# Kernel tuning notes

Hardware: AMD Instinct MI355X
Metric: run time of the kernel (lower is better)

The kernel has to match this reference:

```python
import jax, jax.numpy as jnp
import numpy as np

DIM = 1024
HEADS = 16
DIM_HEAD = 64
INNER = HEADS * DIM_HEAD  # 1024
MAX_POS = 512
B, N = 2, 1024


def setup_inputs() -> dict:
    key = jax.random.key(0)
    ks = jax.random.split(key, 6)
    s = DIM ** -0.5
    x = jax.random.normal(ks[0], (B, N, DIM), dtype=jnp.float32)
    Wq = jax.random.normal(ks[1], (DIM, INNER), dtype=jnp.float32) * s
    Wkv = jax.random.normal(ks[2], (DIM, 2 * INNER), dtype=jnp.float32) * s
    Wo = jax.random.normal(ks[3], (INNER, DIM), dtype=jnp.float32) * (INNER ** -0.5)
    bo = jnp.zeros((DIM,), dtype=jnp.float32)
    rel_emb = jax.random.normal(ks[4], (2 * MAX_POS + 1, DIM_HEAD), dtype=jnp.float32)
    return {"x": x, "Wq": Wq, "Wkv": Wkv, "Wo": Wo, "bo": bo, "rel_emb": rel_emb}


def reference(x, Wq, Wkv, Wo, bo, rel_emb):
    b, n, _ = x.shape
    scale = DIM_HEAD ** -0.5
    q = x @ Wq                    # [b, n, inner]
    kv = x @ Wkv                  # [b, n, 2*inner]
    k, v = jnp.split(kv, 2, axis=-1)

    def split_heads(t):
        return t.reshape(b, n, HEADS, DIM_HEAD).transpose(0, 2, 1, 3)  # [b,h,n,d]

    q, k, v = map(split_heads, (q, k, v))
    dots = jnp.einsum('bhid,bhjd->bhij', q, k) * scale

    seq = jnp.arange(n)
    dist = jnp.clip(seq[:, None] - seq[None, :], -MAX_POS, MAX_POS) + MAX_POS  # [n, n]
    rel = rel_emb[dist]           # [n, n, d]
    pos_attn = jnp.einsum('bhnd,nrd->bhnr', q, rel) * scale
    dots = dots + pos_attn

    attn = jax.nn.softmax(dots, axis=-1)
    out = jnp.einsum('bhij,bhjd->bhid', attn, v)
    out = out.transpose(0, 2, 1, 3).reshape(b, n, INNER)
    return out @ Wo + bo
```

## Files before the change

kernel.cpp:

```cpp
#include <hip/hip_runtime.h>

typedef __bf16 bf16x8 __attribute__((ext_vector_type(8)));
typedef float f32x4 __attribute__((ext_vector_type(4)));

#define DEV __device__ __forceinline__

DEV unsigned short f2bf(float f) {
  union { float f; unsigned u; } x; x.f = f;
  unsigned r = x.u + 0x7FFFu + ((x.u >> 16) & 1u);
  return (unsigned short)(r >> 16);
}
DEV float bf2f(unsigned short h) {
  union { unsigned u; float f; } x; x.u = ((unsigned)h) << 16;
  return x.f;
}

typedef __attribute__((address_space(3))) void* lds_vp;
typedef const __attribute__((address_space(1))) void* gbl_vp;
DEV void load_lds16(const unsigned short* gp, void* lp) {
  __builtin_amdgcn_global_load_lds((gbl_vp)(const void*)gp, (lds_vp)lp, 16, 0, 0);
}

__global__ __launch_bounds__(256)
void prep_k(const float* __restrict__ x, const float* __restrict__ rel,
            const float* __restrict__ bo, const float* __restrict__ Wq,
            const float* __restrict__ Wkv, const float* __restrict__ Wo,
            unsigned short* __restrict__ xb, unsigned short* __restrict__ relb,
            unsigned short* __restrict__ bob, unsigned short* __restrict__ WqkvT,
            unsigned short* __restrict__ WoT) {
  __shared__ unsigned short tile[32][33];
  const int bid = blockIdx.x, tid = threadIdx.x;
  if (bid < 2114) {
    const float* src; unsigned short* dst; long base; long n;
    if (bid < 2048)      { src = x;   dst = xb;   base = (long)bid * 1024;          n = 2097152; }
    else if (bid < 2113) { src = rel; dst = relb; base = (long)(bid - 2048) * 1024; n = 65600; }
    else                 { src = bo;  dst = bob;  base = 0;                          n = 1024; }
    long i = base + tid * 4;
    if (i < n) {
      float4 v = *(const float4*)&src[i];
      unsigned long long u = (unsigned long long)f2bf(v.x)
                           | ((unsigned long long)f2bf(v.y) << 16)
                           | ((unsigned long long)f2bf(v.z) << 32)
                           | ((unsigned long long)f2bf(v.w) << 48);
      *(unsigned long long*)&dst[i] = u;
    }
  } else {
    int id = bid - 2114;
    const float* src; unsigned short* dst; const int R = 1024; int C, txt, tyt;
    if (id < 1024)      { src = Wq;  dst = WqkvT;           C = 1024; txt = id & 31; tyt = id >> 5; }
    else if (id < 3072) { int l = id - 1024; src = Wkv; dst = WqkvT + 1048576; C = 2048; txt = l & 63; tyt = l >> 6; }
    else                { int l = id - 3072; src = Wo;  dst = WoT;             C = 1024; txt = l & 31; tyt = l >> 5; }
    int c0 = txt * 32, r0 = tyt * 32;
    int tx = tid & 31, ty = tid >> 5;
    #pragma unroll
    for (int i = 0; i < 4; ++i)
      tile[ty + i * 8][tx] = f2bf(src[(size_t)(r0 + ty + i * 8) * C + c0 + tx]);
    __syncthreads();
    #pragma unroll
    for (int i = 0; i < 4; ++i)
      dst[(size_t)(c0 + ty + i * 8) * R + r0 + tx] = tile[tx][ty + i * 8];
  }
}

__global__ __launch_bounds__(256)
void gemm_qkv(const unsigned short* __restrict__ A,
              const unsigned short* __restrict__ Bt,
              unsigned short* __restrict__ o0,
              unsigned short* __restrict__ o1,
              unsigned short* __restrict__ o2) {
  __shared__ __align__(16) unsigned short As[128][32];
  __shared__ __align__(16) unsigned short Bs[128][32];
  const int tid  = threadIdx.x;
  const int lane = tid & 63, wave = tid >> 6;
  const int q15  = lane & 15, quad = lane >> 4;
  const int wr = wave >> 1, wc = wave & 1;
  const int m0 = blockIdx.y * 128, n0 = blockIdx.x * 128;
  const int K = 1024;
  const int lrow = lane >> 2, lkc = (lane & 3) * 8;

  f32x4 acc[4][4] = {};
  for (int k0 = 0; k0 < K; k0 += 32) {
    __syncthreads();
    #pragma unroll
    for (int t = 0; t < 2; ++t) {
      int r0 = wave * 32 + t * 16;
      load_lds16(&A[(size_t)(m0 + r0 + lrow) * K + k0 + lkc], &As[r0][0]);
      load_lds16(&Bt[(size_t)(n0 + r0 + lrow) * K + k0 + lkc], &Bs[r0][0]);
    }
    __syncthreads();
    bf16x8 af[4], bfr[4];
    #pragma unroll
    for (int i = 0; i < 4; ++i) {
      af[i]  = *(const bf16x8*)&As[wr * 64 + i * 16 + q15][quad * 8];
      bfr[i] = *(const bf16x8*)&Bs[wc * 64 + i * 16 + q15][quad * 8];
    }
    #pragma unroll
    for (int i = 0; i < 4; ++i)
      #pragma unroll
      for (int j = 0; j < 4; ++j)
        acc[i][j] = __builtin_amdgcn_mfma_f32_16x16x32_bf16(af[i], bfr[j], acc[i][j], 0, 0, 0);
  }
  #pragma unroll
  for (int i = 0; i < 4; ++i)
    #pragma unroll
    for (int j = 0; j < 4; ++j)
      #pragma unroll
      for (int r = 0; r < 4; ++r) {
        int row = m0 + wr * 64 + i * 16 + quad * 4 + r;
        int col = n0 + wc * 64 + j * 16 + q15;
        float v = acc[i][j][r];
        int b = row >> 10, nn = row & 1023;
        unsigned short* dst; int c = col; float sc = 1.f;
        if (col < 1024)      { dst = o0; sc = 0.125f; }
        else if (col < 2048) { dst = o1; c = col - 1024; }
        else                 { dst = o2; c = col - 2048; }
        int h = c >> 6, dd = c & 63;
        dst[((size_t)(b * 16 + h) * 1024 + nn) * 64 + dd] = f2bf(v * sc);
      }
}

__global__ __launch_bounds__(256)
void transpose_v_k(const unsigned short* __restrict__ v,
                   unsigned short* __restrict__ vt) {
  __shared__ __align__(16) unsigned short st[64][68];
  const int bh = blockIdx.y, n0 = blockIdx.x * 64;
  const unsigned short* vp = v + (size_t)bh * 1024 * 64;
  unsigned short* tp = vt + (size_t)bh * 64 * 1024;
  #pragma unroll
  for (int cc = 0; cc < 2; ++cc) {
    int ci = threadIdx.x + cc * 256;
    int row = ci >> 3, dc = (ci & 7) * 8;
    *(uint4*)&st[row][dc] = *(const uint4*)&vp[(size_t)(n0 + row) * 64 + dc];
  }
  __syncthreads();
  #pragma unroll
  for (int cc = 0; cc < 2; ++cc) {
    int ci = threadIdx.x + cc * 256;
    int d = ci >> 3, nc = (ci & 7) * 8;
    union { uint4 v; unsigned short us[8]; } t;
    #pragma unroll
    for (int e = 0; e < 8; ++e) t.us[e] = st[nc + e][d];
    *(uint4*)&tp[(size_t)d * 1024 + n0 + nc] = t.v;
  }
}

DEV void stage16(const unsigned short* gbase, size_t gstride,
                 unsigned short* lbase, int r0, int lane) {
  #pragma unroll
  for (int t = 0; t < 2; ++t) {
    int r = r0 + t * 8 + (lane >> 3);
    int lc = (lane & 7) ^ (r & 7);
    load_lds16(&gbase[(size_t)r * gstride + lc * 8], &lbase[(size_t)(r0 + t * 8) * 64]);
  }
}
DEV bf16x8 read_swz(const unsigned short* buf, int row, int lc) {
  int pc = lc ^ (row & 7);
  return *(const bf16x8*)&buf[row * 64 + pc * 8];
}

__global__ __launch_bounds__(256)
void flash_attn(const unsigned short* __restrict__ q_ws,
                const unsigned short* __restrict__ k_ws,
                const unsigned short* __restrict__ vt_ws,
                const unsigned short* __restrict__ rel,
                unsigned short* __restrict__ Opart,
                float* __restrict__ lpart) {
  __shared__ __align__(16) unsigned short Kbuf[2][64 * 64];
  __shared__ __align__(16) unsigned short Vbuf[2][64 * 64];
  __shared__ __align__(16) unsigned short P_lds[4][16 * 64];

  const int tid  = threadIdx.x;
  const int lane = tid & 63, w = tid >> 6;
  const int q15  = lane & 15, quad = lane >> 4;
  const int bh = blockIdx.x;
  const int it = blockIdx.y >> 1, sp = blockIdx.y & 1;
  const int ib = it * 64 + w * 16;
  const int jbase = sp * 512;

  const unsigned short* qp = q_ws  + (size_t)bh * 1024 * 64;
  const unsigned short* kp = k_ws  + (size_t)bh * 1024 * 64;
  const unsigned short* tp = vt_ws + (size_t)bh * 64 * 1024;

  bf16x8 aq[2];
  #pragma unroll
  for (int ks = 0; ks < 2; ++ks)
    aq[ks] = *(const bf16x8*)&qp[(size_t)(ib + q15) * 64 + ks * 32 + quad * 8];

  f32x4 o[4] = {};
  float l_i[4] = {0.f, 0.f, 0.f, 0.f};

  stage16(kp + (size_t)jbase * 64, 64, &Kbuf[0][0], w * 16, lane);
  stage16(tp + jbase, 1024, &Vbuf[0][0], w * 16, lane);

  for (int jt = 0; jt < 8; ++jt) {
    const int j0 = jbase + jt * 64, cur = jt & 1;
    __syncthreads();
    if (jt + 1 < 8) {
      stage16(kp + (size_t)(j0 + 64) * 64, 64, &Kbuf[cur ^ 1][0], w * 16, lane);
      stage16(tp + (j0 + 64), 1024, &Vbuf[cur ^ 1][0], w * 16, lane);
    }

    f32x4 accS[4] = {};
    #pragma unroll
    for (int ks = 0; ks < 2; ++ks)
      #pragma unroll
      for (int cb = 0; cb < 4; ++cb) {
        bf16x8 bk = read_swz(&Kbuf[cur][0], cb * 16 + q15, ks * 4 + quad);
        accS[cb] = __builtin_amdgcn_mfma_f32_16x16x32_bf16(aq[ks], bk, accS[cb], 0, 0, 0);
      }
    int tb = ib - j0 + 512 - 63;
    f32x4 accT[5] = {};
    #pragma unroll
    for (int ks = 0; ks < 2; ++ks)
      #pragma unroll
      for (int ub = 0; ub < 5; ++ub) {
        int trow = tb + ub * 16 + q15;
        trow = trow < 0 ? 0 : (trow > 1024 ? 1024 : trow);
        bf16x8 br = *(const bf16x8*)&rel[(size_t)trow * 64 + ks * 32 + quad * 8];
        accT[ub] = __builtin_amdgcn_mfma_f32_16x16x32_bf16(aq[ks], br, accT[ub], 0, 0, 0);
      }

    #pragma unroll
    for (int r = 0; r < 4; ++r) {
      const int dl = quad * 4 + r;
      const int src = quad * 16 + ((15 + dl - q15) & 15);
      float tv[5];
      #pragma unroll
      for (int ub = 0; ub < 5; ++ub)
        tv[ub] = __shfl(accT[ub][r], src, 64);
      const bool hi = (q15 < dl);
      #pragma unroll
      for (int cb = 0; cb < 4; ++cb) {
        float tval = hi ? tv[4 - cb] : tv[3 - cb];
        float s = accS[cb][r] + tval;
        float p = exp2f(s * 1.44269504f - 64.f);
        l_i[r] += p;
        int k = cb * 16 + q15;
        P_lds[w][dl * 64 + ((((k >> 3) ^ (dl & 7)) << 3) | (k & 7))] = f2bf(p);
      }
    }

    #pragma unroll
    for (int ks = 0; ks < 2; ++ks) {
      bf16x8 ap = *(const bf16x8*)&P_lds[w][q15 * 64 + (((ks * 4 + quad) ^ (q15 & 7)) << 3)];
      #pragma unroll
      for (int db = 0; db < 4; ++db) {
        bf16x8 bv = read_swz(&Vbuf[cur][0], db * 16 + q15, ks * 4 + quad);
        o[db] = __builtin_amdgcn_mfma_f32_16x16x32_bf16(ap, bv, o[db], 0, 0, 0);
      }
    }
  }

  #pragma unroll
  for (int r = 0; r < 4; ++r)
    #pragma unroll
    for (int off = 1; off < 16; off <<= 1)
      l_i[r] += __shfl_xor(l_i[r], off, 64);

  unsigned short* op = Opart + ((size_t)sp * 32 + bh) * 1024 * 64;
  #pragma unroll
  for (int db = 0; db < 4; ++db)
    #pragma unroll
    for (int r = 0; r < 4; ++r) {
      int row = ib + quad * 4 + r;
      op[(size_t)row * 64 + db * 16 + q15] = f2bf(o[db][r]);
    }
  if (q15 == 0)
    #pragma unroll
    for (int r = 0; r < 4; ++r)
      lpart[(size_t)sp * 32768 + bh * 1024 + ib + quad * 4 + r] = l_i[r];
}

__global__ __launch_bounds__(256)
void combine_k(const unsigned short* __restrict__ Opart,
               const float* __restrict__ lpart,
               unsigned short* __restrict__ ao) {
  int e = (blockIdx.x * 256 + threadIdx.x) * 4;
  if (e >= 2097152) return;
  int bh = e >> 16, rem = e & 65535, row = rem >> 6, d = e & 63;
  size_t off = (size_t)bh * 65536 + rem;
  const unsigned short* p0 = Opart + off;
  const unsigned short* p1 = Opart + 2097152 + off;
  float li = 1.f / (lpart[bh * 1024 + row] + lpart[32768 + bh * 1024 + row] + 1e-30f);
  ushort2 a0 = *(const ushort2*)p0, a1 = *(const ushort2*)(p0 + 2);
  ushort2 b0 = *(const ushort2*)p1, b1 = *(const ushort2*)(p1 + 2);
  int b = bh >> 4, h = bh & 15;
  unsigned short* dst = ao + ((size_t)(b * 1024 + row)) * 1024 + h * 64 + d;
  dst[0] = f2bf((bf2f(a0.x) + bf2f(b0.x)) * li);
  dst[1] = f2bf((bf2f(a0.y) + bf2f(b0.y)) * li);
  dst[2] = f2bf((bf2f(a1.x) + bf2f(b1.x)) * li);
  dst[3] = f2bf((bf2f(a1.y) + bf2f(b1.y)) * li);
}

__global__ __launch_bounds__(256)
void gemm_out(const unsigned short* __restrict__ A,
              const unsigned short* __restrict__ Bt,
              const unsigned short* __restrict__ bias,
              float* __restrict__ fo) {
  __shared__ __align__(16) unsigned short As[128][32];
  __shared__ __align__(16) unsigned short Bs[64][32];
  const int tid  = threadIdx.x;
  const int lane = tid & 63, w = tid >> 6;
  const int q15  = lane & 15, quad = lane >> 4;
  const int m0 = blockIdx.y * 128, n0 = blockIdx.x * 64;
  const int K = 1024, N = 1024;
  const int lrow = lane >> 2, lkc = (lane & 3) * 8;

  f32x4 acc[2][4] = {};
  for (int k0 = 0; k0 < K; k0 += 32) {
    __syncthreads();
    #pragma unroll
    for (int t = 0; t < 2; ++t) {
      int r0 = w * 32 + t * 16;
      load_lds16(&A[(size_t)(m0 + r0 + lrow) * K + k0 + lkc], &As[r0][0]);
    }
    load_lds16(&Bt[(size_t)(n0 + w * 16 + lrow) * K + k0 + lkc], &Bs[w * 16][0]);
    __syncthreads();
    bf16x8 af[2], bfr[4];
    #pragma unroll
    for (int i = 0; i < 2; ++i)
      af[i] = *(const bf16x8*)&As[w * 32 + i * 16 + q15][quad * 8];
    #pragma unroll
    for (int j = 0; j < 4; ++j)
      bfr[j] = *(const bf16x8*)&Bs[j * 16 + q15][quad * 8];
    #pragma unroll
    for (int i = 0; i < 2; ++i)
      #pragma unroll
      for (int j = 0; j < 4; ++j)
        acc[i][j] = __builtin_amdgcn_mfma_f32_16x16x32_bf16(af[i], bfr[j], acc[i][j], 0, 0, 0);
  }
  #pragma unroll
  for (int i = 0; i < 2; ++i)
    #pragma unroll
    for (int j = 0; j < 4; ++j)
      #pragma unroll
      for (int r = 0; r < 4; ++r) {
        int row = m0 + w * 32 + i * 16 + quad * 4 + r;
        int col = n0 + j * 16 + q15;
        fo[(size_t)row * N + col] = acc[i][j][r] + bf2f(bias[col]);
      }
}

extern "C" void kernel_launch(void* const* d_in, const int* in_sizes, int n_in,
                              void* d_out, int out_size, void* d_ws, size_t ws_size,
                              hipStream_t stream) {
  (void)in_sizes; (void)n_in; (void)out_size; (void)ws_size;
  const float* x   = (const float*)d_in[0];
  const float* Wq  = (const float*)d_in[1];
  const float* Wkv = (const float*)d_in[2];
  const float* Wo  = (const float*)d_in[3];
  const float* bo  = (const float*)d_in[4];
  const float* rel = (const float*)d_in[5];
  float* out = (float*)d_out;

  unsigned short* ws = (unsigned short*)d_ws;
  unsigned short* WoT   = ws;
  unsigned short* relb  = WoT   + 1048576;
  unsigned short* bob   = relb  + 65664;
  unsigned short* q_ws  = bob   + 1088;
  unsigned short* k_ws  = q_ws  + 2097152;
  unsigned short* vT    = k_ws  + 2097152;
  unsigned short* WqkvT = vT    + 2097152;
  unsigned short* xb    = WqkvT + 3145728;
  unsigned short* v_row = xb    + 2097152;
  float*          lpart = (float*)(v_row + 2097152);
  unsigned short* Opart = WqkvT;
  unsigned short* ao    = v_row;

  prep_k<<<6210, 256, 0, stream>>>(x, rel, bo, Wq, Wkv, Wo,
                                   xb, relb, bob, WqkvT, WoT);
  gemm_qkv<<<dim3(24, 16), 256, 0, stream>>>(xb, WqkvT, q_ws, k_ws, v_row);
  transpose_v_k<<<dim3(16, 32), 256, 0, stream>>>(v_row, vT);
  flash_attn<<<dim3(32, 32), 256, 0, stream>>>(q_ws, k_ws, vT, relb, Opart, lpart);
  combine_k<<<2048, 256, 0, stream>>>(Opart, lpart, ao);
  gemm_out<<<dim3(16, 16), 256, 0, stream>>>(ao, WoT, bob, out);
}
```

Measured before the change: 189.6 us.

## Fuse V transpose into QKV GEMM epilogue and drop split-KV combine pass

The QKV GEMM epilogue now transposes V tiles through LDS and writes V^T directly, which removes the separate transpose kernel and the row-major V buffer. Flash attention no longer splits the key range in two. Each block loops over all 16 key tiles, normalizes by the row sum, and writes the merged head-interleaved output directly. This eliminates the combine kernel and the partial output and sum-buffer traffic. In exchange the attention grid shrinks to half as many blocks, each doing twice the sequential work, which reduces parallelism on the GPU.

```diff
diff --git a/kernel.cpp b/kernel.cpp
--- a/kernel.cpp
+++ b/kernel.cpp
@@ -70,6 +70,7 @@
               unsigned short* __restrict__ o2) {
   __shared__ __align__(16) unsigned short As[128][32];
   __shared__ __align__(16) unsigned short Bs[128][32];
+  __shared__ unsigned short tbuf[128][68];
   const int tid  = threadIdx.x;
   const int lane = tid & 63, wave = tid >> 6;
   const int q15  = lane & 15, quad = lane >> 4;
@@ -100,47 +101,53 @@
       for (int j = 0; j < 4; ++j)
         acc[i][j] = __builtin_amdgcn_mfma_f32_16x16x32_bf16(af[i], bfr[j], acc[i][j], 0, 0, 0);
   }
-  #pragma unroll
-  for (int i = 0; i < 4; ++i)
-    #pragma unroll
-    for (int j = 0; j < 4; ++j)
-      #pragma unroll
-      for (int r = 0; r < 4; ++r) {
-        int row = m0 + wr * 64 + i * 16 + quad * 4 + r;
-        int col = n0 + wc * 64 + j * 16 + q15;
-        float v = acc[i][j][r];
-        int b = row >> 10, nn = row & 1023;
-        unsigned short* dst; int c = col; float sc = 1.f;
-        if (col < 1024)      { dst = o0; sc = 0.125f; }
-        else if (col < 2048) { dst = o1; c = col - 1024; }
-        else                 { dst = o2; c = col - 2048; }
-        int h = c >> 6, dd = c & 63;
-        dst[((size_t)(b * 16 + h) * 1024 + nn) * 64 + dd] = f2bf(v * sc);
-      }
-}
-
-__global__ __launch_bounds__(256)
-void transpose_v_k(const unsigned short* __restrict__ v,
-                   unsigned short* __restrict__ vt) {
-  __shared__ __align__(16) unsigned short st[64][68];
-  const int bh = blockIdx.y, n0 = blockIdx.x * 64;
-  const unsigned short* vp = v + (size_t)bh * 1024 * 64;
-  unsigned short* tp = vt + (size_t)bh * 64 * 1024;
-  #pragma unroll
-  for (int cc = 0; cc < 2; ++cc) {
-    int ci = threadIdx.x + cc * 256;
-    int row = ci >> 3, dc = (ci & 7) * 8;
-    *(uint4*)&st[row][dc] = *(const uint4*)&vp[(size_t)(n0 + row) * 64 + dc];
-  }
-  __syncthreads();
-  #pragma unroll
-  for (int cc = 0; cc < 2; ++cc) {
-    int ci = threadIdx.x + cc * 256;
-    int d = ci >> 3, nc = (ci & 7) * 8;
-    union { uint4 v; unsigned short us[8]; } t;
-    #pragma unroll
-    for (int e = 0; e < 8; ++e) t.us[e] = st[nc + e][d];
-    *(uint4*)&tp[(size_t)d * 1024 + n0 + nc] = t.v;
+
+  const int b = m0 >> 10, nn0 = m0 & 1023;
+  if (n0 < 2048) {
+    #pragma unroll
+    for (int i = 0; i < 4; ++i)
+      #pragma unroll
+      for (int j = 0; j < 4; ++j)
+        #pragma unroll
+        for (int r = 0; r < 4; ++r) {
+          int row = m0 + wr * 64 + i * 16 + quad * 4 + r;
+          int col = n0 + wc * 64 + j * 16 + q15;
+          float v = acc[i][j][r];
+          int nn = row & 1023;
+          unsigned short* dst; int c = col; float sc = 1.f;
+          if (col < 1024) { dst = o0; sc = 0.125f; }
+          else            { dst = o1; c = col - 1024; }
+          int h = c >> 6, dd = c & 63;
+          dst[((size_t)((row >> 10) * 16 + h) * 1024 + nn) * 64 + dd] = f2bf(v * sc);
+        }
+  } else {
+    const int hp = (n0 - 2048) >> 6;
+    #pragma unroll
+    for (int hh = 0; hh < 2; ++hh) {
+      __syncthreads();
+      if (wc == hh) {
+        #pragma unroll
+        for (int i = 0; i < 4; ++i)
+          #pragma unroll
+          for (int j = 0; j < 4; ++j)
+            #pragma unroll
+            for (int r = 0; r < 4; ++r)
+              tbuf[wr * 64 + i * 16 + quad * 4 + r][j * 16 + q15] = f2bf(acc[i][j][r]);
+      }
+      __syncthreads();
+      const int bh = b * 16 + hp + hh;
+      const int dl = tid >> 3, nb = (tid & 7) * 8;
+      #pragma unroll
+      for (int p = 0; p < 2; ++p)
+        #pragma unroll
+        for (int s = 0; s < 2; ++s) {
+          int d = dl + p * 32, n = nb + s * 64;
+          union { uint4 v; unsigned short us[8]; } t;
+          #pragma unroll
+          for (int e = 0; e < 8; ++e) t.us[e] = tbuf[n + e][d];
+          *(uint4*)&o2[((size_t)bh * 64 + d) * 1024 + nn0 + n] = t.v;
+        }
+    }
   }
 }
 
@@ -163,8 +170,7 @@
                 const unsigned short* __restrict__ k_ws,
                 const unsigned short* __restrict__ vt_ws,
                 const unsigned short* __restrict__ rel,
-                unsigned short* __restrict__ Opart,
-                float* __restrict__ lpart) {
+                unsigned short* __restrict__ ao) {
   __shared__ __align__(16) unsigned short Kbuf[2][64 * 64];
   __shared__ __align__(16) unsigned short Vbuf[2][64 * 64];
   __shared__ __align__(16) unsigned short P_lds[4][16 * 64];
@@ -173,9 +179,7 @@
   const int lane = tid & 63, w = tid >> 6;
   const int q15  = lane & 15, quad = lane >> 4;
   const int bh = blockIdx.x;
-  const int it = blockIdx.y >> 1, sp = blockIdx.y & 1;
-  const int ib = it * 64 + w * 16;
-  const int jbase = sp * 512;
+  const int ib = blockIdx.y * 64 + w * 16;
 
   const unsigned short* qp = q_ws  + (size_t)bh * 1024 * 64;
   const unsigned short* kp = k_ws  + (size_t)bh * 1024 * 64;
@@ -189,13 +193,13 @@
   f32x4 o[4] = {};
   float l_i[4] = {0.f, 0.f, 0.f, 0.f};
 
-  stage16(kp + (size_t)jbase * 64, 64, &Kbuf[0][0], w * 16, lane);
-  stage16(tp + jbase, 1024, &Vbuf[0][0], w * 16, lane);
-
-  for (int jt = 0; jt < 8; ++jt) {
-    const int j0 = jbase + jt * 64, cur = jt & 1;
-    __syncthreads();
-    if (jt + 1 < 8) {
+  stage16(kp, 64, &Kbuf[0][0], w * 16, lane);
+  stage16(tp, 1024, &Vbuf[0][0], w * 16, lane);
+
+  for (int jt = 0; jt < 16; ++jt) {
+    const int j0 = jt * 64, cur = jt & 1;
+    __syncthreads();
+    if (jt + 1 < 16) {
       stage16(kp + (size_t)(j0 + 64) * 64, 64, &Kbuf[cur ^ 1][0], w * 16, lane);
       stage16(tp + (j0 + 64), 1024, &Vbuf[cur ^ 1][0], w * 16, lane);
     }
@@ -252,44 +256,22 @@
   }
 
   #pragma unroll
-  for (int r = 0; r < 4; ++r)
+  for (int r = 0; r < 4; ++r) {
     #pragma unroll
     for (int off = 1; off < 16; off <<= 1)
       l_i[r] += __shfl_xor(l_i[r], off, 64);
-
-  unsigned short* op = Opart + ((size_t)sp * 32 + bh) * 1024 * 64;
+    l_i[r] = 1.f / (l_i[r] + 1e-30f);
+  }
+
+  const int b = bh >> 4, h = bh & 15;
   #pragma unroll
   for (int db = 0; db < 4; ++db)
     #pragma unroll
     for (int r = 0; r < 4; ++r) {
       int row = ib + quad * 4 + r;
-      op[(size_t)row * 64 + db * 16 + q15] = f2bf(o[db][r]);
-    }
-  if (q15 == 0)
-    #pragma unroll
-    for (int r = 0; r < 4; ++r)
-      lpart[(size_t)sp * 32768 + bh * 1024 + ib + quad * 4 + r] = l_i[r];
-}
-
-__global__ __launch_bounds__(256)
-void combine_k(const unsigned short* __restrict__ Opart,
-               const float* __restrict__ lpart,
-               unsigned short* __restrict__ ao) {
-  int e = (blockIdx.x * 256 + threadIdx.x) * 4;
-  if (e >= 2097152) return;
-  int bh = e >> 16, rem = e & 65535, row = rem >> 6, d = e & 63;
-  size_t off = (size_t)bh * 65536 + rem;
-  const unsigned short* p0 = Opart + off;
-  const unsigned short* p1 = Opart + 2097152 + off;
-  float li = 1.f / (lpart[bh * 1024 + row] + lpart[32768 + bh * 1024 + row] + 1e-30f);
-  ushort2 a0 = *(const ushort2*)p0, a1 = *(const ushort2*)(p0 + 2);
-  ushort2 b0 = *(const ushort2*)p1, b1 = *(const ushort2*)(p1 + 2);
-  int b = bh >> 4, h = bh & 15;
-  unsigned short* dst = ao + ((size_t)(b * 1024 + row)) * 1024 + h * 64 + d;
-  dst[0] = f2bf((bf2f(a0.x) + bf2f(b0.x)) * li);
-  dst[1] = f2bf((bf2f(a0.y) + bf2f(b0.y)) * li);
-  dst[2] = f2bf((bf2f(a1.x) + bf2f(b1.x)) * li);
-  dst[3] = f2bf((bf2f(a1.y) + bf2f(b1.y)) * li);
+      ao[((size_t)(b * 1024 + row)) * 1024 + h * 64 + db * 16 + q15] =
+          f2bf(o[db][r] * l_i[r]);
+    }
 }
 
 __global__ __launch_bounds__(256)
@@ -362,16 +344,11 @@
   unsigned short* vT    = k_ws  + 2097152;
   unsigned short* WqkvT = vT    + 2097152;
   unsigned short* xb    = WqkvT + 3145728;
-  unsigned short* v_row = xb    + 2097152;
-  float*          lpart = (float*)(v_row + 2097152);
-  unsigned short* Opart = WqkvT;
-  unsigned short* ao    = v_row;
+  unsigned short* ao    = WqkvT;
 
   prep_k<<<6210, 256, 0, stream>>>(x, rel, bo, Wq, Wkv, Wo,
                                    xb, relb, bob, WqkvT, WoT);
-  gemm_qkv<<<dim3(24, 16), 256, 0, stream>>>(xb, WqkvT, q_ws, k_ws, v_row);
-  transpose_v_k<<<dim3(16, 32), 256, 0, stream>>>(v_row, vT);
-  flash_attn<<<dim3(32, 32), 256, 0, stream>>>(q_ws, k_ws, vT, relb, Opart, lpart);
-  combine_k<<<2048, 256, 0, stream>>>(Opart, lpart, ao);
+  gemm_qkv<<<dim3(24, 16), 256, 0, stream>>>(xb, WqkvT, q_ws, k_ws, vT);
+  flash_attn<<<dim3(32, 16), 256, 0, stream>>>(q_ws, k_ws, vT, relb, ao);
   gemm_out<<<dim3(16, 16), 256, 0, stream>>>(ao, WoT, bob, out);
 }
```

Result: no change. 193.0 us (+1.8%).
